# Kernel tuning notes

Measured on AMD Instinct MI355X. Metric: run time of the kernel, lower is better.

The kernel has to match this reference:

```python
import jax, jax.numpy as jnp
import numpy as np

N, E = 20000, 160000
D_IN, HID, HEADS = 256, 64, 10
NEG_SLOPE = 0.2


def setup_inputs() -> dict:
    key = jax.random.key(0)
    ks = jax.random.split(key, 12)
    s = 0.05
    f = jnp.float32
    return {
        "x": jax.random.normal(ks[0], (N, D_IN), f),
        "edge_index": jax.random.randint(ks[1], (2, E), 0, N, jnp.int32),
        # GATConv 1: in=D_IN, out=HID, heads=10, concat=True
        "W1": (jax.random.normal(ks[2], (D_IN, HEADS * HID), f) * s),
        "a_src1": (jax.random.normal(ks[3], (HEADS, HID), f) * s),
        "a_dst1": (jax.random.normal(ks[4], (HEADS, HID), f) * s),
        "b1": jnp.zeros((HEADS * HID,), f),
        # GATConv 2: in=HEADS*HID, out=HID, heads=1
        "W2": (jax.random.normal(ks[5], (HEADS * HID, HID), f) * s),
        "a_src2": (jax.random.normal(ks[6], (1, HID), f) * s),
        "a_dst2": (jax.random.normal(ks[7], (1, HID), f) * s),
        "b2": jnp.zeros((HID,), f),
        # final Linear(hidden_dim, hidden_dim)
        "Wfc": (jax.random.normal(ks[8], (HID, HID), f) * s),
        "bfc": jnp.zeros((HID,), f),
    }


def gat_conv(x, src, dst, n, W, a_src, a_dst, b, heads, concat):
    """PyG GATConv (eval mode): gather, leaky-relu scores, segment softmax, scatter."""
    c = W.shape[1] // heads
    h = (x @ W).reshape(n, heads, c)                      # [N, H, C]
    score_src = jnp.sum(h * a_src, axis=-1)               # [N, H]
    score_dst = jnp.sum(h * a_dst, axis=-1)               # [N, H]
    e = jax.nn.leaky_relu(score_src[src] + score_dst[dst], NEG_SLOPE)  # [E, H]
    # segment softmax over incoming edges of each dst node
    m = jax.ops.segment_max(e, dst, num_segments=n)
    e = jnp.exp(e - m[dst])
    denom = jax.ops.segment_sum(e, dst, num_segments=n)
    alpha = e / (denom[dst] + 1e-16)                      # [E, H]
    msg = alpha[:, :, None] * h[src]                      # [E, H, C]
    out = jax.ops.segment_sum(msg, dst, num_segments=n)   # [N, H, C]
    out = out.reshape(n, heads * c) if concat else out.mean(axis=1)
    return out + b


def reference(x, edge_index, W1, a_src1, a_dst1, b1, W2, a_src2, a_dst2, b2, Wfc, bfc):
    n = x.shape[0]
    # add self loops (PyG default)
    loops = jnp.arange(n, dtype=edge_index.dtype)
    src = jnp.concatenate([edge_index[0], loops])
    dst = jnp.concatenate([edge_index[1], loops])
    h = jax.nn.relu(gat_conv(x, src, dst, n, W1, a_src1, a_dst1, b1, HEADS, True))
    h = jax.nn.relu(gat_conv(h, src, dst, n, W2, a_src2, a_dst2, b2, 1, True))
    return jax.nn.relu(h @ Wfc + bfc)
```

## Files before the change

kernel.cpp:

```cpp
#include <hip/hip_runtime.h>
#include <cstdint>
#include <cstddef>

constexpr int N_NODES = 20000;
constexpr int E_EDGES = 160000;
constexpr int D_INC   = 256;
constexpr int HEADSC  = 10;
constexpr int EN      = E_EDGES + N_NODES;
constexpr int ELLW    = 96;
constexpr float NEG_SLOPE = 0.2f;

typedef _Float16 half8 __attribute__((ext_vector_type(8)));
typedef _Float16 half4v __attribute__((ext_vector_type(4)));
typedef float f32x4 __attribute__((ext_vector_type(4)));

#define GLOBAL_AS const __attribute__((address_space(1))) void*
#define LDS_AS __attribute__((address_space(3))) void*

__global__ __launch_bounds__(256) void gemm1_k(
    const float* __restrict__ X,
    const _Float16* __restrict__ BT,
    _Float16* __restrict__ C,
    const float* __restrict__ asv, const float* __restrict__ adv,
    float* __restrict__ s_s, float* __restrict__ s_d, int M)
{
    __shared__ alignas(16) _Float16 Ah[64][68];
    __shared__ alignas(16) _Float16 Bh[128][64];
    const int tid = threadIdx.x;
    const int wv  = tid >> 6;
    const int ln  = tid & 63;
    const int row0 = blockIdx.y * 64;
    const int col0 = blockIdx.x * 128;
    const int m = ln & 15;
    const int q = ln >> 4;
    const int ar = ln >> 3;
    const int ac = (ln & 7) * 8;
    const int arow = tid >> 2;
    const int acg  = (tid & 3) * 16;

    f32x4 acc[8] = {};

    for (int k0 = 0; k0 < 256; k0 += 64) {
        float4 v0 = make_float4(0.f, 0.f, 0.f, 0.f), v1 = v0, v2 = v0, v3 = v0;
        if (row0 + arow < M) {
            const float* xp = X + (size_t)(row0 + arow) * 256 + k0 + acg;
            v0 = *reinterpret_cast<const float4*>(xp);
            v1 = *reinterpret_cast<const float4*>(xp + 4);
            v2 = *reinterpret_cast<const float4*>(xp + 8);
            v3 = *reinterpret_cast<const float4*>(xp + 12);
        }
        half8 h0 = {(_Float16)v0.x, (_Float16)v0.y, (_Float16)v0.z, (_Float16)v0.w,
                    (_Float16)v1.x, (_Float16)v1.y, (_Float16)v1.z, (_Float16)v1.w};
        half8 h1v = {(_Float16)v2.x, (_Float16)v2.y, (_Float16)v2.z, (_Float16)v2.w,
                     (_Float16)v3.x, (_Float16)v3.y, (_Float16)v3.z, (_Float16)v3.w};
        *reinterpret_cast<half8*>(&Ah[arow][acg])     = h0;
        *reinterpret_cast<half8*>(&Ah[arow][acg + 8]) = h1v;
        const _Float16* gb = BT + (size_t)(col0 + wv * 32 + ar) * 256 + k0 + ac;
#pragma unroll
        for (int jj = 0; jj < 4; ++jj) {
            __builtin_amdgcn_global_load_lds((GLOBAL_AS)(gb + (size_t)jj * 8 * 256),
                                             (LDS_AS)&Bh[wv * 32 + jj * 8][0],
                                             16, 0, 0);
        }
        __syncthreads();
#pragma unroll
        for (int ks = 0; ks < 2; ++ks) {
            const half8 af = *reinterpret_cast<const half8*>(
                &Ah[wv * 16 + m][ks * 32 + q * 8]);
#pragma unroll
            for (int ct = 0; ct < 8; ++ct) {
                const half8 bf = *reinterpret_cast<const half8*>(
                    &Bh[ct * 16 + m][ks * 32 + q * 8]);
                acc[ct] = __builtin_amdgcn_mfma_f32_16x16x32_f16(af, bf, acc[ct],
                                                                 0, 0, 0);
            }
        }
        __syncthreads();
    }

#pragma unroll
    for (int ct = 0; ct < 8; ++ct) {
#pragma unroll
        for (int r = 0; r < 4; ++r) {
            const int row = row0 + wv * 16 + q * 4 + r;
            if (row < M)
                C[(size_t)row * 640 + col0 + ct * 16 + m] = (_Float16)acc[ct][r];
        }
    }

    const int h0i = blockIdx.x * 2;
    float pa[2][4] = {}, pd[2][4] = {};
#pragma unroll
    for (int ct = 0; ct < 8; ++ct) {
        const int hh = ct >> 2;
        const int ch = (ct & 3) * 16 + m;
        const float a_ = asv[(h0i + hh) * 64 + ch];
        const float d_ = adv[(h0i + hh) * 64 + ch];
#pragma unroll
        for (int r = 0; r < 4; ++r) {
            pa[hh][r] += acc[ct][r] * a_;
            pd[hh][r] += acc[ct][r] * d_;
        }
    }
#pragma unroll
    for (int o = 1; o < 16; o <<= 1) {
#pragma unroll
        for (int hh = 0; hh < 2; ++hh)
#pragma unroll
            for (int r = 0; r < 4; ++r) {
                pa[hh][r] += __shfl_xor(pa[hh][r], o, 64);
                pd[hh][r] += __shfl_xor(pd[hh][r], o, 64);
            }
    }
    if (m == 0) {
#pragma unroll
        for (int hh = 0; hh < 2; ++hh)
#pragma unroll
            for (int r = 0; r < 4; ++r) {
                const int row = row0 + wv * 16 + q * 4 + r;
                if (row < M) {
                    s_s[row * HEADSC + h0i + hh] = pa[hh][r];
                    s_d[row * HEADSC + h0i + hh] = pd[hh][r];
                }
            }
    }
}

__global__ __launch_bounds__(256) void gemm2_k(
    const _Float16* __restrict__ A,
    const _Float16* __restrict__ BT,
    _Float16* __restrict__ C,
    const float* __restrict__ asv, const float* __restrict__ adv,
    float* __restrict__ s_s, float* __restrict__ s_d, int M)
{
    __shared__ alignas(16) _Float16 Ah[64][64];
    __shared__ alignas(16) _Float16 Bh[64][64];
    const int tid = threadIdx.x;
    const int wv  = tid >> 6;
    const int ln  = tid & 63;
    const int row0 = blockIdx.x * 64;
    const int m = ln & 15;
    const int q = ln >> 4;
    const int ar = ln >> 3;
    const int ac = (ln & 7) * 8;

    f32x4 acc[4] = {};

    for (int k0 = 0; k0 < 640; k0 += 64) {
        const _Float16* gp0 = A + (size_t)(row0 + wv * 16 + ar) * 640 + k0 + ac;
        __builtin_amdgcn_global_load_lds((GLOBAL_AS)gp0,
                                         (LDS_AS)&Ah[wv * 16][0], 16, 0, 0);
        __builtin_amdgcn_global_load_lds((GLOBAL_AS)(gp0 + 8 * 640),
                                         (LDS_AS)&Ah[wv * 16 + 8][0], 16, 0, 0);
        const _Float16* gb = BT + (size_t)(wv * 16 + ar) * 640 + k0 + ac;
        __builtin_amdgcn_global_load_lds((GLOBAL_AS)gb,
                                         (LDS_AS)&Bh[wv * 16][0], 16, 0, 0);
        __builtin_amdgcn_global_load_lds((GLOBAL_AS)(gb + 8 * 640),
                                         (LDS_AS)&Bh[wv * 16 + 8][0], 16, 0, 0);
        __syncthreads();
#pragma unroll
        for (int ks = 0; ks < 2; ++ks) {
            const half8 af = *reinterpret_cast<const half8*>(
                &Ah[wv * 16 + m][ks * 32 + q * 8]);
#pragma unroll
            for (int ct = 0; ct < 4; ++ct) {
                const half8 bf = *reinterpret_cast<const half8*>(
                    &Bh[ct * 16 + m][ks * 32 + q * 8]);
                acc[ct] = __builtin_amdgcn_mfma_f32_16x16x32_f16(af, bf, acc[ct],
                                                                 0, 0, 0);
            }
        }
        __syncthreads();
    }

#pragma unroll
    for (int ct = 0; ct < 4; ++ct) {
#pragma unroll
        for (int r = 0; r < 4; ++r) {
            const int row = row0 + wv * 16 + q * 4 + r;
            if (row < M)
                C[(size_t)row * 64 + ct * 16 + m] = (_Float16)acc[ct][r];
        }
    }

    float pa[4] = {}, pd[4] = {};
#pragma unroll
    for (int ct = 0; ct < 4; ++ct) {
        const float a_ = asv[ct * 16 + m];
        const float d_ = adv[ct * 16 + m];
#pragma unroll
        for (int r = 0; r < 4; ++r) {
            pa[r] += acc[ct][r] * a_;
            pd[r] += acc[ct][r] * d_;
        }
    }
#pragma unroll
    for (int o = 1; o < 16; o <<= 1) {
#pragma unroll
        for (int r = 0; r < 4; ++r) {
            pa[r] += __shfl_xor(pa[r], o, 64);
            pd[r] += __shfl_xor(pd[r], o, 64);
        }
    }
    if (m == 0) {
#pragma unroll
        for (int r = 0; r < 4; ++r) {
            const int row = row0 + wv * 16 + q * 4 + r;
            if (row < M) { s_s[row] = pa[r]; s_d[row] = pd[r]; }
        }
    }
}

constexpr int W1E  = D_INC * 640;
constexpr int W2E  = 640 * 64;
constexpr int WFCE = 64 * 64;
constexpr int SETUP_TOT = EN + W1E + W2E + WFCE;

__global__ void setup_k(const int* __restrict__ src, const int* __restrict__ dst,
                        int* __restrict__ deg, int* __restrict__ ell,
                        const float* __restrict__ W1, const float* __restrict__ W2,
                        const float* __restrict__ Wfc,
                        _Float16* __restrict__ W1T, _Float16* __restrict__ W2T,
                        _Float16* __restrict__ WfcT)
{
    const int i = blockIdx.x * 256 + threadIdx.x;
    if (i < EN) {
        const int base = deg[N_NODES];
        int d, s;
        if (i < E_EDGES) { d = dst[i]; s = src[i]; }
        else             { d = i - E_EDGES; s = d; }
        const int r = atomicAdd(&deg[d], 1) - base;
        if ((unsigned)r < (unsigned)ELLW) ell[(size_t)d * ELLW + r] = s;
    } else if (i < EN + W1E) {
        const int j = i - EN;
        const int k = j / 640, n = j - k * 640;
        W1T[(size_t)n * D_INC + k] = (_Float16)W1[j];
    } else if (i < EN + W1E + W2E) {
        const int j = i - EN - W1E;
        const int k = j / 64, n = j - k * 64;
        W2T[(size_t)n * 640 + k] = (_Float16)W2[j];
    } else if (i < SETUP_TOT) {
        const int j = i - EN - W1E - W2E;
        const int k = j >> 6, n = j & 63;
        WfcT[(size_t)n * 64 + k] = (_Float16)Wfc[j];
    }
}

__global__ __launch_bounds__(320) void agg_f16_oct(
    const _Float16* __restrict__ h, const float* __restrict__ s_s,
    const float* __restrict__ s_d, const int* __restrict__ deg,
    const int* __restrict__ ell, const float* __restrict__ bias,
    _Float16* __restrict__ outp, int n_base)
{
    const int t   = blockIdx.x * 320 + threadIdx.x;
    const int n   = n_base + t / 80;
    const int oct = t - (t / 80) * 80;
    if (n >= N_NODES) return;
    const int hh  = oct >> 3;
    const _Float16* __restrict__ hb = h + oct * 8;
    const int* __restrict__ row = ell + (size_t)n * ELLW;
    const float sd = s_d[n * HEADSC + hh];
    const int dbase = deg[N_NODES];
    const int dc = min(deg[n] - dbase, ELLW);

    float acc[8] = {};
    float den = 0.f;
    int i = 0;
    for (; i + 3 < dc; i += 4) {
        const int s0 = row[i], s1 = row[i + 1], s2 = row[i + 2], s3 = row[i + 3];
        const float g0 = s_s[s0 * HEADSC + hh], g1 = s_s[s1 * HEADSC + hh];
        const float g2 = s_s[s2 * HEADSC + hh], g3 = s_s[s3 * HEADSC + hh];
        const half8 v0 = *reinterpret_cast<const half8*>(hb + (size_t)s0 * 640);
        const half8 v1 = *reinterpret_cast<const half8*>(hb + (size_t)s1 * 640);
        const half8 v2 = *reinterpret_cast<const half8*>(hb + (size_t)s2 * 640);
        const half8 v3 = *reinterpret_cast<const half8*>(hb + (size_t)s3 * 640);
        float e0 = g0 + sd, e1 = g1 + sd, e2 = g2 + sd, e3 = g3 + sd;
        e0 = (e0 > 0.f) ? e0 : NEG_SLOPE * e0;
        e1 = (e1 > 0.f) ? e1 : NEG_SLOPE * e1;
        e2 = (e2 > 0.f) ? e2 : NEG_SLOPE * e2;
        e3 = (e3 > 0.f) ? e3 : NEG_SLOPE * e3;
        const float w0 = __expf(e0), w1 = __expf(e1);
        const float w2 = __expf(e2), w3 = __expf(e3);
        den += (w0 + w1) + (w2 + w3);
#pragma unroll
        for (int j = 0; j < 8; ++j)
            acc[j] += (w0 * (float)v0[j] + w1 * (float)v1[j])
                    + (w2 * (float)v2[j] + w3 * (float)v3[j]);
    }
    for (; i < dc; ++i) {
        const int s0 = row[i];
        const float g0 = s_s[s0 * HEADSC + hh];
        const half8 v0 = *reinterpret_cast<const half8*>(hb + (size_t)s0 * 640);
        float e0 = g0 + sd;
        e0 = (e0 > 0.f) ? e0 : NEG_SLOPE * e0;
        const float w0 = __expf(e0);
        den += w0;
#pragma unroll
        for (int j = 0; j < 8; ++j) acc[j] += w0 * (float)v0[j];
    }
    const float inv = 1.f / (den + 1e-16f);
    const float* bb = bias + oct * 8;
    half8 o;
#pragma unroll
    for (int j = 0; j < 8; ++j)
        o[j] = (_Float16)fmaxf(acc[j] * inv + bb[j], 0.f);
    *reinterpret_cast<half8*>(outp + (size_t)n * 640 + oct * 8) = o;
}

__global__ __launch_bounds__(256) void agg2fc_k(
    const _Float16* __restrict__ h,
    const float* __restrict__ s_s, const float* __restrict__ s_d,
    const int* __restrict__ deg, const int* __restrict__ ell,
    const float* __restrict__ b2,
    const _Float16* __restrict__ WfcT,
    const float* __restrict__ bfc,
    float* __restrict__ out)
{
    __shared__ alignas(16) _Float16 Os[32][72];
    const int tid = threadIdx.x;
    const int n0  = blockIdx.x * 32;
    const int nl  = tid >> 3;
    const int oct = tid & 7;
    const int n   = n0 + nl;

    {
        const _Float16* __restrict__ hb = h + oct * 8;
        const int* __restrict__ row = ell + (size_t)n * ELLW;
        const float sd = s_d[n];
        const int dbase = deg[N_NODES];
        const int dc = min(deg[n] - dbase, ELLW);

        float acc[8] = {};
        float den = 0.f;
        int i = 0;
        for (; i + 3 < dc; i += 4) {
            int   sv[4];
            float gv[4];
            half8 hv[4];
#pragma unroll
            for (int u = 0; u < 4; ++u) sv[u] = row[i + u];
#pragma unroll
            for (int u = 0; u < 4; ++u) gv[u] = s_s[sv[u]];
#pragma unroll
            for (int u = 0; u < 4; ++u)
                hv[u] = *reinterpret_cast<const half8*>(hb + (size_t)sv[u] * 64);
#pragma unroll
            for (int u = 0; u < 4; ++u) {
                float e = gv[u] + sd;
                e = (e > 0.f) ? e : NEG_SLOPE * e;
                const float w = __expf(e);
                den += w;
#pragma unroll
                for (int j = 0; j < 8; ++j) acc[j] += w * (float)hv[u][j];
            }
        }
        for (; i < dc; ++i) {
            const int s0 = row[i];
            const float g0 = s_s[s0];
            const half8 v0 = *reinterpret_cast<const half8*>(hb + (size_t)s0 * 64);
            float e0 = g0 + sd;
            e0 = (e0 > 0.f) ? e0 : NEG_SLOPE * e0;
            const float w0 = __expf(e0);
            den += w0;
#pragma unroll
            for (int j = 0; j < 8; ++j) acc[j] += w0 * (float)v0[j];
        }
        const float inv = 1.f / (den + 1e-16f);
        const float* bb = b2 + oct * 8;
        half8 o;
#pragma unroll
        for (int j = 0; j < 8; ++j)
            o[j] = (_Float16)fmaxf(acc[j] * inv + bb[j], 0.f);
        *reinterpret_cast<half8*>(&Os[nl][oct * 8]) = o;
    }
    __syncthreads();

    const int wv = tid >> 6;
    const int ln = tid & 63;
    if (wv < 2) {
        const int m = ln & 15;
        const int q = ln >> 4;
        f32x4 acc[4] = {};
#pragma unroll
        for (int ks = 0; ks < 2; ++ks) {
            const half8 af = *reinterpret_cast<const half8*>(
                &Os[wv * 16 + m][ks * 32 + q * 8]);
#pragma unroll
            for (int ct = 0; ct < 4; ++ct) {
                const half8 bf = *reinterpret_cast<const half8*>(
                    WfcT + (size_t)(ct * 16 + m) * 64 + ks * 32 + q * 8);
                acc[ct] = __builtin_amdgcn_mfma_f32_16x16x32_f16(af, bf, acc[ct],
                                                                 0, 0, 0);
            }
        }
#pragma unroll
        for (int ct = 0; ct < 4; ++ct) {
#pragma unroll
            for (int r = 0; r < 4; ++r) {
                const int row = n0 + wv * 16 + q * 4 + r;
                const int col = ct * 16 + m;
                out[(size_t)row * 64 + col] = fmaxf(acc[ct][r] + bfc[col], 0.f);
            }
        }
    }
}

extern "C" void kernel_launch(void* const* d_in, const int* in_sizes, int n_in,
                              void* d_out, int out_size, void* d_ws, size_t ws_size,
                              hipStream_t stream)
{
    const float* x      = (const float*)d_in[0];
    const int*   edges  = (const int*)d_in[1];
    const float* W1     = (const float*)d_in[2];
    const float* a_src1 = (const float*)d_in[3];
    const float* a_dst1 = (const float*)d_in[4];
    const float* b1     = (const float*)d_in[5];
    const float* W2     = (const float*)d_in[6];
    const float* a_src2 = (const float*)d_in[7];
    const float* a_dst2 = (const float*)d_in[8];
    const float* b2     = (const float*)d_in[9];
    const float* Wfc    = (const float*)d_in[10];
    const float* bfc    = (const float*)d_in[11];
    float* out = (float*)d_out;

    const int* src = edges;
    const int* dst = edges + E_EDGES;

    char* ws = (char*)d_ws;
    size_t off = 0;
    auto alloc = [&](size_t bytes) -> void* {
        void* p = ws + off;
        off += (bytes + 255) & ~(size_t)255;
        return p;
    };
    _Float16*  h1     = (_Float16*)alloc((size_t)N_NODES * 640 * sizeof(_Float16));
    _Float16*  out1   = (_Float16*)alloc((size_t)N_NODES * 640 * sizeof(_Float16));
    _Float16*  h2     = (_Float16*)alloc((size_t)N_NODES * 64 * sizeof(_Float16));
    _Float16*  W1T    = (_Float16*)alloc((size_t)640 * D_INC * sizeof(_Float16));
    _Float16*  W2T    = (_Float16*)alloc((size_t)64 * 640 * sizeof(_Float16));
    _Float16*  WfcT   = (_Float16*)alloc((size_t)64 * 64 * sizeof(_Float16));
    float*     s_src1 = (float*)alloc((size_t)N_NODES * HEADSC * sizeof(float));
    float*     s_dst1 = (float*)alloc((size_t)N_NODES * HEADSC * sizeof(float));
    float*     s_src2 = (float*)alloc((size_t)N_NODES * sizeof(float));
    float*     s_dst2 = (float*)alloc((size_t)N_NODES * sizeof(float));
    int*       deg    = (int*)alloc((size_t)(N_NODES + 1) * sizeof(int));
    int*       ell    = (int*)alloc((size_t)N_NODES * ELLW * sizeof(int));

    setup_k<<<(SETUP_TOT + 255) / 256, 256, 0, stream>>>(
        src, dst, deg, ell, W1, W2, Wfc, W1T, W2T, WfcT);

    dim3 g1(5, (N_NODES + 63) / 64);
    gemm1_k<<<g1, 256, 0, stream>>>(x, W1T, h1, a_src1, a_dst1,
                                    s_src1, s_dst1, N_NODES);

    agg_f16_oct<<<2500, 320, 0, stream>>>(h1, s_src1, s_dst1, deg, ell, b1,
                                          out1, 0);
    agg_f16_oct<<<2500, 320, 0, stream>>>(h1, s_src1, s_dst1, deg, ell, b1,
                                          out1, 10000);

    gemm2_k<<<(N_NODES + 63) / 64, 256, 0, stream>>>(out1, W2T, h2,
                                                     a_src2, a_dst2,
                                                     s_src2, s_dst2, N_NODES);

    agg2fc_k<<<N_NODES / 32, 256, 0, stream>>>(h2, s_src2, s_dst2, deg, ell,
                                               b2, WfcT, bfc, out);
}
```

Measured before the change: 196.4 us.

## Register-prefetch next K tile in both GEMMs and shrink gemm2 block tile

Both GEMM kernels stop using direct global-to-LDS loads. Each thread now prefetches the next K slice into registers while the MFMA work on the current slice runs, then writes it to LDS at the top of the next iteration. LDS rows are padded to 72 halves to cut bank conflicts. gemm2 moves from 64-row, 256-thread blocks to 32-row, 128-thread blocks, giving 625 blocks, and drops its row bounds checks since N divides evenly by 32. The cost is higher register use and an extra register-to-LDS copy.

```diff
diff --git a/kernel.cpp b/kernel.cpp
--- a/kernel.cpp
+++ b/kernel.cpp
@@ -11,11 +11,7 @@
 constexpr float NEG_SLOPE = 0.2f;
 
 typedef _Float16 half8 __attribute__((ext_vector_type(8)));
-typedef _Float16 half4v __attribute__((ext_vector_type(4)));
 typedef float f32x4 __attribute__((ext_vector_type(4)));
-
-#define GLOBAL_AS const __attribute__((address_space(1))) void*
-#define LDS_AS __attribute__((address_space(3))) void*
 
 __global__ __launch_bounds__(256) void gemm1_k(
     const float* __restrict__ X,
@@ -24,8 +20,8 @@
     const float* __restrict__ asv, const float* __restrict__ adv,
     float* __restrict__ s_s, float* __restrict__ s_d, int M)
 {
-    __shared__ alignas(16) _Float16 Ah[64][68];
-    __shared__ alignas(16) _Float16 Bh[128][64];
+    __shared__ alignas(16) _Float16 Ah[64][72];
+    __shared__ alignas(16) _Float16 Bh[128][72];
     const int tid = threadIdx.x;
     const int wv  = tid >> 6;
     const int ln  = tid & 63;
@@ -33,36 +29,59 @@
     const int col0 = blockIdx.x * 128;
     const int m = ln & 15;
     const int q = ln >> 4;
-    const int ar = ln >> 3;
-    const int ac = (ln & 7) * 8;
     const int arow = tid >> 2;
     const int acg  = (tid & 3) * 16;
+    const int brow = tid >> 1;
+    const int bcg  = (tid & 1) * 32;
+
+    const bool aok = (row0 + arow) < M;
+    const float*    xrow = X  + (size_t)(row0 + arow) * 256 + acg;
+    const _Float16* bptr = BT + (size_t)(col0 + brow) * 256 + bcg;
+
+    float4 av0, av1, av2, av3;
+    int4   bv0, bv1, bv2, bv3;
+    av0 = av1 = av2 = av3 = make_float4(0.f, 0.f, 0.f, 0.f);
+    if (aok) {
+        av0 = *reinterpret_cast<const float4*>(xrow);
+        av1 = *reinterpret_cast<const float4*>(xrow + 4);
+        av2 = *reinterpret_cast<const float4*>(xrow + 8);
+        av3 = *reinterpret_cast<const float4*>(xrow + 12);
+    }
+    bv0 = *reinterpret_cast<const int4*>(bptr);
+    bv1 = *reinterpret_cast<const int4*>(bptr + 8);
+    bv2 = *reinterpret_cast<const int4*>(bptr + 16);
+    bv3 = *reinterpret_cast<const int4*>(bptr + 24);
 
     f32x4 acc[8] = {};
 
     for (int k0 = 0; k0 < 256; k0 += 64) {
-        float4 v0 = make_float4(0.f, 0.f, 0.f, 0.f), v1 = v0, v2 = v0, v3 = v0;
-        if (row0 + arow < M) {
-            const float* xp = X + (size_t)(row0 + arow) * 256 + k0 + acg;
-            v0 = *reinterpret_cast<const float4*>(xp);
-            v1 = *reinterpret_cast<const float4*>(xp + 4);
-            v2 = *reinterpret_cast<const float4*>(xp + 8);
-            v3 = *reinterpret_cast<const float4*>(xp + 12);
-        }
-        half8 h0 = {(_Float16)v0.x, (_Float16)v0.y, (_Float16)v0.z, (_Float16)v0.w,
-                    (_Float16)v1.x, (_Float16)v1.y, (_Float16)v1.z, (_Float16)v1.w};
-        half8 h1v = {(_Float16)v2.x, (_Float16)v2.y, (_Float16)v2.z, (_Float16)v2.w,
-                     (_Float16)v3.x, (_Float16)v3.y, (_Float16)v3.z, (_Float16)v3.w};
+        half8 h0 = {(_Float16)av0.x, (_Float16)av0.y, (_Float16)av0.z, (_Float16)av0.w,
+                    (_Float16)av1.x, (_Float16)av1.y, (_Float16)av1.z, (_Float16)av1.w};
+        half8 h1v = {(_Float16)av2.x, (_Float16)av2.y, (_Float16)av2.z, (_Float16)av2.w,
+                     (_Float16)av3.x, (_Float16)av3.y, (_Float16)av3.z, (_Float16)av3.w};
         *reinterpret_cast<half8*>(&Ah[arow][acg])     = h0;
         *reinterpret_cast<half8*>(&Ah[arow][acg + 8]) = h1v;
-        const _Float16* gb = BT + (size_t)(col0 + wv * 32 + ar) * 256 + k0 + ac;
-#pragma unroll
-        for (int jj = 0; jj < 4; ++jj) {
-            __builtin_amdgcn_global_load_lds((GLOBAL_AS)(gb + (size_t)jj * 8 * 256),
-                                             (LDS_AS)&Bh[wv * 32 + jj * 8][0],
-                                             16, 0, 0);
-        }
+        *reinterpret_cast<int4*>(&Bh[brow][bcg])      = bv0;
+        *reinterpret_cast<int4*>(&Bh[brow][bcg + 8])  = bv1;
+        *reinterpret_cast<int4*>(&Bh[brow][bcg + 16]) = bv2;
+        *reinterpret_cast<int4*>(&Bh[brow][bcg + 24]) = bv3;
         __syncthreads();
+
+        if (k0 + 64 < 256) {
+            const float* xp = xrow + k0 + 64;
+            if (aok) {
+                av0 = *reinterpret_cast<const float4*>(xp);
+                av1 = *reinterpret_cast<const float4*>(xp + 4);
+                av2 = *reinterpret_cast<const float4*>(xp + 8);
+                av3 = *reinterpret_cast<const float4*>(xp + 12);
+            }
+            const _Float16* bp = bptr + k0 + 64;
+            bv0 = *reinterpret_cast<const int4*>(bp);
+            bv1 = *reinterpret_cast<const int4*>(bp + 8);
+            bv2 = *reinterpret_cast<const int4*>(bp + 16);
+            bv3 = *reinterpret_cast<const int4*>(bp + 24);
+        }
+
 #pragma unroll
         for (int ks = 0; ks < 2; ++ks) {
             const half8 af = *reinterpret_cast<const half8*>(
@@ -126,38 +145,59 @@
     }
 }
 
-__global__ __launch_bounds__(256) void gemm2_k(
+__global__ __launch_bounds__(128) void gemm2_k(
     const _Float16* __restrict__ A,
     const _Float16* __restrict__ BT,
     _Float16* __restrict__ C,
     const float* __restrict__ asv, const float* __restrict__ adv,
-    float* __restrict__ s_s, float* __restrict__ s_d, int M)
+    float* __restrict__ s_s, float* __restrict__ s_d)
 {
-    __shared__ alignas(16) _Float16 Ah[64][64];
-    __shared__ alignas(16) _Float16 Bh[64][64];
+    __shared__ alignas(16) _Float16 Ah[32][72];
+    __shared__ alignas(16) _Float16 Bh[64][72];
     const int tid = threadIdx.x;
     const int wv  = tid >> 6;
     const int ln  = tid & 63;
-    const int row0 = blockIdx.x * 64;
+    const int row0 = blockIdx.x * 32;
     const int m = ln & 15;
     const int q = ln >> 4;
-    const int ar = ln >> 3;
-    const int ac = (ln & 7) * 8;
+    const int arow = tid >> 2;
+    const int acg  = (tid & 3) * 16;
+    const int brow = tid >> 1;
+    const int bcg  = (tid & 1) * 32;
+
+    const _Float16* aptr = A  + (size_t)(row0 + arow) * 640 + acg;
+    const _Float16* bptr = BT + (size_t)brow * 640 + bcg;
+
+    int4 a0, a1, b0, b1, b2, b3;
+    a0 = *reinterpret_cast<const int4*>(aptr);
+    a1 = *reinterpret_cast<const int4*>(aptr + 8);
+    b0 = *reinterpret_cast<const int4*>(bptr);
+    b1 = *reinterpret_cast<const int4*>(bptr + 8);
+    b2 = *reinterpret_cast<const int4*>(bptr + 16);
+    b3 = *reinterpret_cast<const int4*>(bptr + 24);
 
     f32x4 acc[4] = {};
 
     for (int k0 = 0; k0 < 640; k0 += 64) {
-        const _Float16* gp0 = A + (size_t)(row0 + wv * 16 + ar) * 640 + k0 + ac;
-        __builtin_amdgcn_global_load_lds((GLOBAL_AS)gp0,
-                                         (LDS_AS)&Ah[wv * 16][0], 16, 0, 0);
-        __builtin_amdgcn_global_load_lds((GLOBAL_AS)(gp0 + 8 * 640),
-                                         (LDS_AS)&Ah[wv * 16 + 8][0], 16, 0, 0);
-        const _Float16* gb = BT + (size_t)(wv * 16 + ar) * 640 + k0 + ac;
-        __builtin_amdgcn_global_load_lds((GLOBAL_AS)gb,
-                                         (LDS_AS)&Bh[wv * 16][0], 16, 0, 0);
-        __builtin_amdgcn_global_load_lds((GLOBAL_AS)(gb + 8 * 640),
-                                         (LDS_AS)&Bh[wv * 16 + 8][0], 16, 0, 0);
+        *reinterpret_cast<int4*>(&Ah[arow][acg])      = a0;
+        *reinterpret_cast<int4*>(&Ah[arow][acg + 8])  = a1;
+        *reinterpret_cast<int4*>(&Bh[brow][bcg])      = b0;
+        *reinterpret_cast<int4*>(&Bh[brow][bcg + 8])  = b1;
+        *reinterpret_cast<int4*>(&Bh[brow][bcg + 16]) = b2;
+        *reinterpret_cast<int4*>(&Bh[brow][bcg + 24]) = b3;
         __syncthreads();
+
+        if (k0 + 64 < 640) {
+            const _Float16* ap = aptr + k0 + 64;
+            a0 = *reinterpret_cast<const int4*>(ap);
+            a1 = *reinterpret_cast<const int4*>(ap + 8);
+            const _Float16* bp = bptr + k0 + 64;
+            b0 = *reinterpret_cast<const int4*>(bp);
+            b1 = *reinterpret_cast<const int4*>(bp + 8);
+            b2 = *reinterpret_cast<const int4*>(bp + 16);
+            b3 = *reinterpret_cast<const int4*>(bp + 24);
+        }
+
 #pragma unroll
         for (int ks = 0; ks < 2; ++ks) {
             const half8 af = *reinterpret_cast<const half8*>(
@@ -178,8 +218,7 @@
 #pragma unroll
         for (int r = 0; r < 4; ++r) {
             const int row = row0 + wv * 16 + q * 4 + r;
-            if (row < M)
-                C[(size_t)row * 64 + ct * 16 + m] = (_Float16)acc[ct][r];
+            C[(size_t)row * 64 + ct * 16 + m] = (_Float16)acc[ct][r];
         }
     }
 
@@ -206,7 +245,8 @@
 #pragma unroll
         for (int r = 0; r < 4; ++r) {
             const int row = row0 + wv * 16 + q * 4 + r;
-            if (row < M) { s_s[row] = pa[r]; s_d[row] = pd[r]; }
+            s_s[row] = pa[r];
+            s_d[row] = pd[r];
         }
     }
 }
@@ -458,9 +498,8 @@
     agg_f16_oct<<<2500, 320, 0, stream>>>(h1, s_src1, s_dst1, deg, ell, b1,
                                           out1, 10000);
 
-    gemm2_k<<<(N_NODES + 63) / 64, 256, 0, stream>>>(out1, W2T, h2,
-                                                     a_src2, a_dst2,
-                                                     s_src2, s_dst2, N_NODES);
+    gemm2_k<<<N_NODES / 32, 128, 0, stream>>>(out1, W2T, h2, a_src2, a_dst2,
+                                              s_src2, s_dst2);
 
     agg2fc_k<<<N_NODES / 32, 256, 0, stream>>>(h2, s_src2, s_dst2, deg, ell,
                                                b2, WfcT, bfc, out);
```

Result: faster. 187.4 us (-4.6%).
